# Performance work log

Hardware: AMD Instinct MI355X
Metric: run time of the kernel (lower is better)

The kernel has to match this reference:

```python
import jax, jax.numpy as jnp
import numpy as np

B = 131072      # batch size
H = 300         # hidden_dim (per-source), se has 2*H = 600 columns
T = 2           # num_source_tasks
EPS = 1e-20


def setup_inputs() -> dict:
    key = jax.random.key(0)
    k1, k2, k3, k4, k5 = jax.random.split(key, 5)
    return {
        "se1": jax.random.normal(k1, (B, H), dtype=jnp.float32),
        "se2": jax.random.normal(k2, (B, H), dtype=jnp.float32),
        "W": jax.random.normal(k3, (T, 2 * H), dtype=jnp.float32) / np.sqrt(2 * H).astype(np.float32),
        "b": jax.random.normal(k4, (T,), dtype=jnp.float32),
        "u": jax.random.uniform(k5, (B, T), dtype=jnp.float32),
        "n_tasks": 2,
    }


def reference(se1, se2, W, b, u, n_tasks):
    # se = torch.cat(se, dim=1) -> [B, 2H]
    se = jnp.concatenate([se1, se2], axis=1)
    # tiny linear + relu + log_softmax
    se_postrelu = jax.nn.relu(se @ W.T + b)            # [B, T]
    logits = jax.nn.log_softmax(se_postrelu, axis=1)   # [B, T]
    # straight-through gumbel-softmax (temperature=1.0, no mask)
    gumbel = -jnp.log(-jnp.log(u + EPS) + EPS)
    y = jax.nn.softmax(logits + gumbel, axis=1)        # soft probs
    y_hard = jax.nn.one_hot(jnp.argmax(y, axis=1), T, dtype=y.dtype)
    selector = jax.lax.stop_gradient(y_hard - y) + y   # ST estimator, [B, T]
    # rf: first H cols = selector[:,0], next H cols = selector[:,1]
    rf = jnp.repeat(selector, H, axis=1)               # [B, 2H]
    return se * rf
```

## Files before the change

### kernel.cpp

```cpp
#include <hip/hip_runtime.h>
#include <math.h>

typedef float f4 __attribute__((ext_vector_type(4)));

#define BDIM 256
#define TROWS 16
#define RPW 4
#define TILE_F4_IN 1200
#define TILE_F4_OUT 2400

__device__ __forceinline__ float dot4(f4 a, f4 w) {
    return a[0]*w[0] + a[1]*w[1] + a[2]*w[2] + a[3]*w[3];
}

__global__ __launch_bounds__(BDIM) void taskselector_kernel(
    const f4* __restrict__ se1,
    const f4* __restrict__ se2,
    const float* __restrict__ W,
    const float* __restrict__ bvec,
    const f4* __restrict__ u4,
    f4* __restrict__ out)
{
    __shared__ f4 L1[TILE_F4_IN];
    __shared__ f4 L2[TILE_F4_IN];
    __shared__ float SEL[TROWS * 2];
    __shared__ f4 UL[TROWS / 2];

    const int tid  = threadIdx.x;
    const int lane = tid & 63;
    const int wave = tid >> 6;
    const int tile = blockIdx.x;

    const bool extra = (lane < 11);
    const f4 zero = (f4)0.f;
    const f4* W0 = (const f4*)W;
    const f4* W1 = (const f4*)(W + 600);
    f4 w0a = W0[lane];
    f4 w0b = extra ? W0[64 + lane]  : zero;
    f4 w0c = W0[75 + lane];
    f4 w0d = extra ? W0[139 + lane] : zero;
    f4 w1a = W1[lane];
    f4 w1b = extra ? W1[64 + lane]  : zero;
    f4 w1c = W1[75 + lane];
    f4 w1d = extra ? W1[139 + lane] : zero;
    const float b0 = bvec[0];
    const float b1 = bvec[1];

    const f4* s1 = se1 + (size_t)tile * TILE_F4_IN;
    const f4* s2 = se2 + (size_t)tile * TILE_F4_IN;
    f4 t[4], q[4];
    #pragma unroll
    for (int k = 0; k < 4; k++) t[k] = __builtin_nontemporal_load(s1 + k * BDIM + tid);
    #pragma unroll
    for (int k = 0; k < 4; k++) q[k] = __builtin_nontemporal_load(s2 + k * BDIM + tid);
    f4 t4 = zero, q4 = zero;
    if (tid < TILE_F4_IN - 4 * BDIM) {
        t4 = __builtin_nontemporal_load(s1 + 4 * BDIM + tid);
        q4 = __builtin_nontemporal_load(s2 + 4 * BDIM + tid);
    }
    if (tid < TROWS / 2) UL[tid] = u4[(size_t)tile * (TROWS / 2) + tid];
    #pragma unroll
    for (int k = 0; k < 4; k++) L1[k * BDIM + tid] = t[k];
    #pragma unroll
    for (int k = 0; k < 4; k++) L2[k * BDIM + tid] = q[k];
    if (tid < TILE_F4_IN - 4 * BDIM) {
        L1[4 * BDIM + tid] = t4;
        L2[4 * BDIM + tid] = q4;
    }
    __syncthreads();

    const float* ULf = (const float*)UL;
    #pragma unroll
    for (int rr = 0; rr < RPW; rr++) {
        const int r = wave * RPW + rr;
        const f4* R1 = L1 + r * 75;
        const f4* R2 = L2 + r * 75;
        f4 a0 = R1[lane];
        f4 c0 = R2[lane];
        f4 a1 = extra ? R1[64 + lane] : zero;
        f4 c1 = extra ? R2[64 + lane] : zero;
        float d0 = dot4(a0, w0a) + dot4(a1, w0b) + dot4(c0, w0c) + dot4(c1, w0d);
        float d1 = dot4(a0, w1a) + dot4(a1, w1b) + dot4(c0, w1c) + dot4(c1, w1d);
        #pragma unroll
        for (int off = 32; off > 0; off >>= 1) {
            d0 += __shfl_xor(d0, off, 64);
            d1 += __shfl_xor(d1, off, 64);
        }
        float z0 = fmaxf(d0 + b0, 0.f);
        float z1 = fmaxf(d1 + b1, 0.f);
        float m  = fmaxf(z0, z1);
        float lse = m + logf(expf(z0 - m) + expf(z1 - m));
        float uu0 = ULf[2 * r];
        float uu1 = ULf[2 * r + 1];
        float q0 = (z0 - lse) + (-logf(-logf(uu0 + 1e-20f) + 1e-20f));
        float q1 = (z1 - lse) + (-logf(-logf(uu1 + 1e-20f) + 1e-20f));
        float mm = fmaxf(q0, q1);
        float e0 = expf(q0 - mm);
        float e1 = expf(q1 - mm);
        float s  = e0 + e1;
        float y0 = e0 / s;
        float y1 = e1 / s;
        bool  pick0 = (q0 >= q1);
        float s0 = pick0 ? ((1.f - y0) + y0) : 0.f;
        float s1v = pick0 ? 0.f : ((1.f - y1) + y1);
        if (lane == 0) { SEL[2 * r] = s0; SEL[2 * r + 1] = s1v; }
    }
    __syncthreads();

    f4* o = out + (size_t)tile * TILE_F4_OUT;
    #pragma unroll
    for (int k = 0; k < 9; k++) {
        const int j   = k * BDIM + tid;
        const int row = j / 150;
        const int rem = j - row * 150;
        const bool first = (rem < 75);
        f4 v = first ? L1[row * 75 + rem] : L2[row * 75 + rem - 75];
        float sc = SEL[2 * row + (first ? 0 : 1)];
        __builtin_nontemporal_store(v * sc, o + j);
    }
    if (tid < TILE_F4_OUT - 9 * BDIM) {
        const int j   = 9 * BDIM + tid;
        const int row = j / 150;
        const int rem = j - row * 150;
        const bool first = (rem < 75);
        f4 v = first ? L1[row * 75 + rem] : L2[row * 75 + rem - 75];
        float sc = SEL[2 * row + (first ? 0 : 1)];
        __builtin_nontemporal_store(v * sc, o + j);
    }
}

extern "C" void kernel_launch(void* const* d_in, const int* in_sizes, int n_in,
                              void* d_out, int out_size, void* d_ws, size_t ws_size,
                              hipStream_t stream) {
    const f4* se1 = (const f4*)d_in[0];
    const f4* se2 = (const f4*)d_in[1];
    const float* W = (const float*)d_in[2];
    const float* b = (const float*)d_in[3];
    const f4* u4  = (const f4*)d_in[4];
    f4* out = (f4*)d_out;

    const int Brows = in_sizes[0] / 300;
    const int ntiles = Brows / TROWS;

    taskselector_kernel<<<ntiles, BDIM, 0, stream>>>(se1, se2, W, b, u4, out);
}
```

Before: 111.3 us.

## Load input rows directly into LDS per wave and drop block barriers

Each wave now owns its four rows and uses global_load_lds to copy se1/se2 straight into its private LDS slice, skipping the register round-trip. The selector values stay in registers and u is read per wave, so both __syncthreads barriers and the shared SEL/UL buffers go away. The risks are that the global_load_lds path drops the nontemporal hint, and that correctness depends on s_waitcnt vmcnt(0) being enough to make the LDS writes visible to the wave.

```diff
diff --git a/kernel.cpp b/kernel.cpp
--- a/kernel.cpp
+++ b/kernel.cpp
@@ -4,10 +4,17 @@
 typedef float f4 __attribute__((ext_vector_type(4)));
 
 #define BDIM 256
-#define TROWS 16
+#define WPB 4
 #define RPW 4
-#define TILE_F4_IN 1200
-#define TILE_F4_OUT 2400
+#define ROWS_PER_BLOCK (WPB * RPW)
+#define WAVE_F4 300
+
+typedef __attribute__((address_space(1))) const unsigned int glob_u32;
+typedef __attribute__((address_space(3))) unsigned int lds_u32;
+
+__device__ __forceinline__ void gload16(const f4* g, f4* l) {
+    __builtin_amdgcn_global_load_lds((glob_u32*)g, (lds_u32*)l, 16, 0, 0);
+}
 
 __device__ __forceinline__ float dot4(f4 a, f4 w) {
     return a[0]*w[0] + a[1]*w[1] + a[2]*w[2] + a[3]*w[3];
@@ -21,15 +28,25 @@
     const f4* __restrict__ u4,
     f4* __restrict__ out)
 {
-    __shared__ f4 L1[TILE_F4_IN];
-    __shared__ f4 L2[TILE_F4_IN];
-    __shared__ float SEL[TROWS * 2];
-    __shared__ f4 UL[TROWS / 2];
+    __shared__ f4 L1[WPB][WAVE_F4];
+    __shared__ f4 L2[WPB][WAVE_F4];
 
     const int tid  = threadIdx.x;
     const int lane = tid & 63;
     const int wave = tid >> 6;
-    const int tile = blockIdx.x;
+    const int rowbase = blockIdx.x * ROWS_PER_BLOCK + wave * RPW;
+
+    f4* Lw1 = &L1[wave][0];
+    f4* Lw2 = &L2[wave][0];
+
+    const f4* g1 = se1 + (size_t)rowbase * 75;
+    const f4* g2 = se2 + (size_t)rowbase * 75;
+    #pragma unroll
+    for (int k = 0; k < 4; k++) gload16(g1 + k * 64 + lane, Lw1 + k * 64);
+    if (lane < 44)              gload16(g1 + 256 + lane,    Lw1 + 256);
+    #pragma unroll
+    for (int k = 0; k < 4; k++) gload16(g2 + k * 64 + lane, Lw2 + k * 64);
+    if (lane < 44)              gload16(g2 + 256 + lane,    Lw2 + 256);
 
     const bool extra = (lane < 11);
     const f4 zero = (f4)0.f;
@@ -45,40 +62,19 @@
     f4 w1d = extra ? W1[139 + lane] : zero;
     const float b0 = bvec[0];
     const float b1 = bvec[1];
+    const f4 ua = u4[rowbase / 2];
+    const f4 ub = u4[rowbase / 2 + 1];
 
-    const f4* s1 = se1 + (size_t)tile * TILE_F4_IN;
-    const f4* s2 = se2 + (size_t)tile * TILE_F4_IN;
-    f4 t[4], q[4];
+    asm volatile("s_waitcnt vmcnt(0)" ::: "memory");
+
+    float s0r[1], dummy; (void)dummy; (void)s0r;
+    float sA0, sA1, sB0, sB1, sC0, sC1, sD0, sD1;
     #pragma unroll
-    for (int k = 0; k < 4; k++) t[k] = __builtin_nontemporal_load(s1 + k * BDIM + tid);
-    #pragma unroll
-    for (int k = 0; k < 4; k++) q[k] = __builtin_nontemporal_load(s2 + k * BDIM + tid);
-    f4 t4 = zero, q4 = zero;
-    if (tid < TILE_F4_IN - 4 * BDIM) {
-        t4 = __builtin_nontemporal_load(s1 + 4 * BDIM + tid);
-        q4 = __builtin_nontemporal_load(s2 + 4 * BDIM + tid);
-    }
-    if (tid < TROWS / 2) UL[tid] = u4[(size_t)tile * (TROWS / 2) + tid];
-    #pragma unroll
-    for (int k = 0; k < 4; k++) L1[k * BDIM + tid] = t[k];
-    #pragma unroll
-    for (int k = 0; k < 4; k++) L2[k * BDIM + tid] = q[k];
-    if (tid < TILE_F4_IN - 4 * BDIM) {
-        L1[4 * BDIM + tid] = t4;
-        L2[4 * BDIM + tid] = q4;
-    }
-    __syncthreads();
-
-    const float* ULf = (const float*)UL;
-    #pragma unroll
-    for (int rr = 0; rr < RPW; rr++) {
-        const int r = wave * RPW + rr;
-        const f4* R1 = L1 + r * 75;
-        const f4* R2 = L2 + r * 75;
-        f4 a0 = R1[lane];
-        f4 c0 = R2[lane];
-        f4 a1 = extra ? R1[64 + lane] : zero;
-        f4 c1 = extra ? R2[64 + lane] : zero;
+    for (int r = 0; r < RPW; r++) {
+        f4 a0 = Lw1[r * 75 + lane];
+        f4 c0 = Lw2[r * 75 + lane];
+        f4 a1 = extra ? Lw1[r * 75 + 64 + lane] : zero;
+        f4 c1 = extra ? Lw2[r * 75 + 64 + lane] : zero;
         float d0 = dot4(a0, w0a) + dot4(a1, w0b) + dot4(c0, w0c) + dot4(c1, w0d);
         float d1 = dot4(a0, w1a) + dot4(a1, w1b) + dot4(c0, w1c) + dot4(c1, w1d);
         #pragma unroll
@@ -90,8 +86,8 @@
         float z1 = fmaxf(d1 + b1, 0.f);
         float m  = fmaxf(z0, z1);
         float lse = m + logf(expf(z0 - m) + expf(z1 - m));
-        float uu0 = ULf[2 * r];
-        float uu1 = ULf[2 * r + 1];
+        float uu0 = (r < 2) ? ((r == 0) ? ua[0] : ua[2]) : ((r == 2) ? ub[0] : ub[2]);
+        float uu1 = (r < 2) ? ((r == 0) ? ua[1] : ua[3]) : ((r == 2) ? ub[1] : ub[3]);
         float q0 = (z0 - lse) + (-logf(-logf(uu0 + 1e-20f) + 1e-20f));
         float q1 = (z1 - lse) + (-logf(-logf(uu1 + 1e-20f) + 1e-20f));
         float mm = fmaxf(q0, q1);
@@ -102,29 +98,25 @@
         float y1 = e1 / s;
         bool  pick0 = (q0 >= q1);
         float s0 = pick0 ? ((1.f - y0) + y0) : 0.f;
-        float s1v = pick0 ? 0.f : ((1.f - y1) + y1);
-        if (lane == 0) { SEL[2 * r] = s0; SEL[2 * r + 1] = s1v; }
+        float s1 = pick0 ? 0.f : ((1.f - y1) + y1);
+        if (r == 0) { sA0 = s0; sA1 = s1; }
+        else if (r == 1) { sB0 = s0; sB1 = s1; }
+        else if (r == 2) { sC0 = s0; sC1 = s1; }
+        else { sD0 = s0; sD1 = s1; }
     }
-    __syncthreads();
 
-    f4* o = out + (size_t)tile * TILE_F4_OUT;
+    f4* o = out + (size_t)rowbase * 150;
     #pragma unroll
-    for (int k = 0; k < 9; k++) {
-        const int j   = k * BDIM + tid;
+    for (int k = 0; k < 10; k++) {
+        const int j = k * 64 + lane;
+        if (k == 9 && lane >= 24) break;
         const int row = j / 150;
         const int rem = j - row * 150;
         const bool first = (rem < 75);
-        f4 v = first ? L1[row * 75 + rem] : L2[row * 75 + rem - 75];
-        float sc = SEL[2 * row + (first ? 0 : 1)];
-        __builtin_nontemporal_store(v * sc, o + j);
-    }
-    if (tid < TILE_F4_OUT - 9 * BDIM) {
-        const int j   = 9 * BDIM + tid;
-        const int row = j / 150;
-        const int rem = j - row * 150;
-        const bool first = (rem < 75);
-        f4 v = first ? L1[row * 75 + rem] : L2[row * 75 + rem - 75];
-        float sc = SEL[2 * row + (first ? 0 : 1)];
+        f4 v = first ? Lw1[row * 75 + rem] : Lw2[row * 75 + rem - 75];
+        float sf = (row < 2) ? ((row == 0) ? sA0 : sB0) : ((row == 2) ? sC0 : sD0);
+        float ss = (row < 2) ? ((row == 0) ? sA1 : sB1) : ((row == 2) ? sC1 : sD1);
+        float sc = first ? sf : ss;
         __builtin_nontemporal_store(v * sc, o + j);
     }
 }
@@ -140,7 +132,7 @@
     f4* out = (f4*)d_out;
 
     const int Brows = in_sizes[0] / 300;
-    const int ntiles = Brows / TROWS;
+    const int nblocks = Brows / ROWS_PER_BLOCK;
 
-    taskselector_kernel<<<ntiles, BDIM, 0, stream>>>(se1, se2, W, b, u4, out);
+    taskselector_kernel<<<nblocks, BDIM, 0, stream>>>(se1, se2, W, b, u4, out);
 }
```

Result: slower. 128.0 us (+15.0%).
